# Optimization experiments

Measured on AMD Instinct MI355X. Metric: run time of the kernel, lower is better.

## Reference

```python
import jax, jax.numpy as jnp
import numpy as np

DIM = 1024
NUM_HEADS = 16
HEAD_DIM = DIM // NUM_HEADS
SCALE = HEAD_DIM ** -0.5


def setup_inputs() -> dict:
    key = jax.random.key(0)
    k1, k2, k3, k4 = jax.random.split(key, 4)
    x = jax.random.normal(k1, (4, 2048, DIM), dtype=jnp.float32)
    # torch nn.Linear(dim, 3*dim, bias=False): weight shape [3*dim, dim]
    w_qkv = jax.random.normal(k2, (3 * DIM, DIM), dtype=jnp.float32) * (DIM ** -0.5)
    # torch nn.Linear(dim, dim): weight [dim, dim], bias [dim]
    w_proj = jax.random.normal(k3, (DIM, DIM), dtype=jnp.float32) * (DIM ** -0.5)
    b_proj = jax.random.normal(k4, (DIM,), dtype=jnp.float32) * 0.01
    return {"x": x, "w_qkv": w_qkv, "w_proj": w_proj, "b_proj": b_proj}


def reference(x, w_qkv, w_proj, b_proj):
    B, N, C = x.shape
    # qkv: [B, N, 3*C] -> [3, B, H, N, Dh]
    qkv = (x @ w_qkv.T).reshape(B, N, 3, NUM_HEADS, HEAD_DIM)
    qkv = jnp.transpose(qkv, (2, 0, 3, 1, 4))
    q, k, v = qkv[0], qkv[1], qkv[2]
    # full score matrix, as in the original module
    attn = jnp.einsum("bhqd,bhkd->bhqk", q, k) * SCALE
    attn = jax.nn.softmax(attn, axis=-1)
    out = jnp.einsum("bhqk,bhkd->bhqd", attn, v)  # [B,H,N,Dh]
    out = jnp.transpose(out, (0, 2, 1, 3)).reshape(B, N, C)
    return out @ w_proj.T + b_proj
```

## Files before the change

### kernel.cpp

```cpp
#include <hip/hip_runtime.h>
#include <stdint.h>

#define DIM 1024
#define SEQ 2048
#define BATCH 4
#define ROWS (BATCH*SEQ)
#define QSCALE 0.1803368801111f

typedef __attribute__((ext_vector_type(8))) short bf16x8;
typedef __attribute__((ext_vector_type(4))) float f32x4;
typedef __attribute__((ext_vector_type(8))) _Float16 f16x8;
typedef __attribute__((ext_vector_type(2))) __fp16 fp16x2_raw;

#if __has_builtin(__builtin_amdgcn_exp2f)
#define EXP2F(x) __builtin_amdgcn_exp2f(x)
#else
#define EXP2F(x) __expf((x) * 0.69314718056f)
#endif

#define MFMA_BF16_K32(a,b,c) __builtin_amdgcn_mfma_f32_16x16x32_bf16(a,b,c,0,0,0)
#define MFMA_F16_K32(a,b,c)  __builtin_amdgcn_mfma_f32_16x16x32_f16(a,b,c,0,0,0)

__device__ __forceinline__ unsigned short f2bf(float f) {
  union { float f; unsigned int u; } v; v.f = f;
  unsigned int u = v.u;
  return (unsigned short)((u + 0x7FFFu + ((u >> 16) & 1u)) >> 16);
}

__device__ __forceinline__ unsigned short f2h(float f) {
  union { _Float16 h; unsigned short u; } v;
  v.h = (_Float16)f;
  return v.u;
}

__device__ __forceinline__ unsigned int pkrtz_bits(float lo, float hi) {
  union { fp16x2_raw h; unsigned int u; } v;
  v.h = __builtin_amdgcn_cvt_pkrtz(lo, hi);
  return v.u;
}

__device__ __forceinline__ void gload_lds16(const void* g, void* l) {
  __builtin_amdgcn_global_load_lds(
      (const __attribute__((address_space(1))) unsigned int*)g,
      (__attribute__((address_space(3))) unsigned int*)l,
      16, 0, 0);
}

__global__ void cast_all(const float* __restrict__ x,
                         const float* __restrict__ wq,
                         const float* __restrict__ wp,
                         unsigned short* __restrict__ xb,
                         unsigned short* __restrict__ wqb,
                         unsigned short* __restrict__ wpb) {
  const int i = (blockIdx.x * blockDim.x + threadIdx.x) * 4;
  const float* src;
  unsigned short* dst;
  int off;
  if (i < ROWS * DIM)                 { src = x;  dst = xb;  off = i; }
  else if (i < ROWS * DIM + 3 * DIM * DIM) { src = wq; dst = wqb; off = i - ROWS * DIM; }
  else                                { src = wp; dst = wpb; off = i - ROWS * DIM - 3 * DIM * DIM; }
  float4 f = *(const float4*)(src + off);
  ushort4 o;
  o.x = f2bf(f.x); o.y = f2bf(f.y); o.z = f2bf(f.z); o.w = f2bf(f.w);
  *(ushort4*)(dst + off) = o;
}

template<int SWAP>
__device__ __forceinline__ f32x4 mm(bf16x8 a, bf16x8 b, f32x4 c) {
  if constexpr (SWAP) return __builtin_amdgcn_mfma_f32_16x16x32_bf16(b, a, c, 0, 0, 0);
  else                return __builtin_amdgcn_mfma_f32_16x16x32_bf16(a, b, c, 0, 0, 0);
}

template<int SWAP, int NTX>
__global__ __launch_bounds__(512, 2) void gemm_qkv8(
    const unsigned short* __restrict__ A,
    const unsigned short* __restrict__ W,
    unsigned short* __restrict__ qb,
    unsigned short* __restrict__ kb,
    unsigned short* __restrict__ vtb) {
  constexpr int K = DIM;
  constexpr int NT = K / 64;
  constexpr int N0B = SWAP ? 0 : 2048;
  __shared__ unsigned short Al[2][256 * 64];
  __shared__ unsigned short Bl[2][256 * 64];

  const int tid  = threadIdx.x;
  const int wave = tid >> 6, lane = tid & 63;
  const int quad = lane >> 4, l16 = lane & 15;
  const int wm = wave >> 2, wn = wave & 3;

  constexpr int nwg = NTX * 32;
  int id = blockIdx.y * NTX + blockIdx.x;
  id = (id & 7) * (nwg >> 3) + (id >> 3);
  const int bx = id % NTX, by = id / NTX;
  const int m0 = by * 256, n0 = N0B + bx * 256;

  const int srow8 = lane >> 3;
  const int schk  = (lane & 7) ^ srow8;
  const unsigned short* Ast = A + (size_t)(m0 + wave * 8 + srow8) * K + (schk << 3);
  const unsigned short* Bst = W + (size_t)(n0 + wave * 8 + srow8) * K + (schk << 3);

  auto stg = [&](const unsigned short* g, int R0, int kt, unsigned short* l) {
    gload_lds16((const void*)(g + (size_t)R0 * K + kt),
                (void*)(l + (R0 + wave * 8) * 64));
  };
  auto ldf = [&](const unsigned short* base, int rb, int idx, int kk) -> bf16x8 {
    const int r = rb + idx * 16 + l16;
    return *(const bf16x8*)&base[r * 64 + (((kk * 4 + quad) ^ (l16 & 7)) << 3)];
  };

  f32x4 acc[8][4];
#pragma unroll
  for (int i = 0; i < 8; ++i)
#pragma unroll
    for (int j = 0; j < 4; ++j) acc[i][j] = (f32x4)0.f;

  stg(Ast, 0, 0, Al[0]);  stg(Ast, 128, 0, Al[0]);
  stg(Ast, 64, 0, Al[0]); stg(Ast, 192, 0, Al[0]);
  stg(Bst, 0, 0, Bl[0]);  stg(Bst, 64, 0, Bl[0]);
  stg(Bst, 128, 0, Bl[0]); stg(Bst, 192, 0, Bl[0]);
  stg(Ast, 0, 64, Al[1]);  stg(Ast, 128, 64, Al[1]);
  stg(Bst, 0, 64, Bl[1]);  stg(Bst, 64, 64, Bl[1]);
  stg(Ast, 64, 64, Al[1]); stg(Ast, 192, 64, Al[1]);
  asm volatile("s_waitcnt vmcnt(6)" ::: "memory");
  __builtin_amdgcn_s_barrier();

  bf16x8 af[4][2], bf[4][2];
  int buf = 0;
  for (int t = 0; t < NT; ++t, buf ^= 1) {
    const unsigned short* Ac = Al[buf];
    const unsigned short* Bc = Bl[buf];
    unsigned short* Asg = Al[buf];
    unsigned short* Bsg = Bl[buf];
    const int kt2 = (t + 2) * 64;

#pragma unroll
    for (int mi = 0; mi < 4; ++mi) {
      af[mi][0] = ldf(Ac, wm * 128, mi, 0);
      af[mi][1] = ldf(Ac, wm * 128, mi, 1);
    }
#pragma unroll
    for (int ni = 0; ni < 2; ++ni) {
      bf[ni][0] = ldf(Bc, wn * 64, ni, 0);
      bf[ni][1] = ldf(Bc, wn * 64, ni, 1);
    }
    if (t + 1 < NT) {
      stg(Bst, 128, (t + 1) * 64, Bl[buf ^ 1]);
      stg(Bst, 192, (t + 1) * 64, Bl[buf ^ 1]);
    }
    __builtin_amdgcn_s_barrier();
    asm volatile("s_waitcnt lgkmcnt(0)" ::: "memory");
    __builtin_amdgcn_s_setprio(1);
#pragma unroll
    for (int mi = 0; mi < 4; ++mi)
#pragma unroll
      for (int ni = 0; ni < 2; ++ni)
#pragma unroll
        for (int kk = 0; kk < 2; ++kk)
          acc[mi][ni] = mm<SWAP>(af[mi][kk], bf[ni][kk], acc[mi][ni]);
    __builtin_amdgcn_s_setprio(0);
    __builtin_amdgcn_s_barrier();

#pragma unroll
    for (int ni = 2; ni < 4; ++ni) {
      bf[ni][0] = ldf(Bc, wn * 64, ni, 0);
      bf[ni][1] = ldf(Bc, wn * 64, ni, 1);
    }
    if (t + 2 < NT) {
      stg(Ast, 0, kt2, Asg);
      stg(Ast, 128, kt2, Asg);
    }
    __builtin_amdgcn_s_barrier();
    asm volatile("s_waitcnt lgkmcnt(0)" ::: "memory");
    __builtin_amdgcn_s_setprio(1);
#pragma unroll
    for (int mi = 0; mi < 4; ++mi)
#pragma unroll
      for (int ni = 2; ni < 4; ++ni)
#pragma unroll
        for (int kk = 0; kk < 2; ++kk)
          acc[mi][ni] = mm<SWAP>(af[mi][kk], bf[ni][kk], acc[mi][ni]);
    __builtin_amdgcn_s_setprio(0);
    __builtin_amdgcn_s_barrier();

#pragma unroll
    for (int mi = 0; mi < 4; ++mi) {
      af[mi][0] = ldf(Ac, wm * 128, mi + 4, 0);
      af[mi][1] = ldf(Ac, wm * 128, mi + 4, 1);
    }
    if (t + 2 < NT) {
      stg(Bst, 0, kt2, Bsg);
      stg(Bst, 64, kt2, Bsg);
    }
    __builtin_amdgcn_s_barrier();
    asm volatile("s_waitcnt lgkmcnt(0)" ::: "memory");
    __builtin_amdgcn_s_setprio(1);
#pragma unroll
    for (int mi = 0; mi < 4; ++mi)
#pragma unroll
      for (int ni = 2; ni < 4; ++ni)
#pragma unroll
        for (int kk = 0; kk < 2; ++kk)
          acc[mi + 4][ni] = mm<SWAP>(af[mi][kk], bf[ni][kk], acc[mi + 4][ni]);
    __builtin_amdgcn_s_setprio(0);
    __builtin_amdgcn_s_barrier();

    if (t + 2 < NT) {
      stg(Ast, 64, kt2, Asg);
      stg(Ast, 192, kt2, Asg);
      asm volatile("s_waitcnt vmcnt(6)" ::: "memory");
    } else {
      asm volatile("s_waitcnt vmcnt(0)" ::: "memory");
    }
    __builtin_amdgcn_s_barrier();
    __builtin_amdgcn_s_setprio(1);
#pragma unroll
    for (int mi = 0; mi < 4; ++mi)
#pragma unroll
      for (int ni = 0; ni < 2; ++ni)
#pragma unroll
        for (int kk = 0; kk < 2; ++kk)
          acc[mi + 4][ni] = mm<SWAP>(af[mi][kk], bf[ni][kk], acc[mi + 4][ni]);
    __builtin_amdgcn_s_setprio(0);
    __builtin_amdgcn_s_barrier();
  }

  if constexpr (SWAP) {
    const float sc = (n0 < 1024) ? QSCALE : 1.f;
    unsigned short* base = (n0 < 1024) ? qb : kb;
#pragma unroll
    for (int mi = 0; mi < 8; ++mi) {
      const int tok = m0 + wm * 128 + mi * 16 + l16;
      const int b = tok >> 11, n = tok & 2047;
#pragma unroll
      for (int ni = 0; ni < 4; ++ni) {
        const int f0 = n0 + wn * 64 + ni * 16 + quad * 4;
        const int h = (f0 >> 6) & 15, d = f0 & 63;
        ushort4 o4;
        o4.x = f2bf(acc[mi][ni][0] * sc);
        o4.y = f2bf(acc[mi][ni][1] * sc);
        o4.z = f2bf(acc[mi][ni][2] * sc);
        o4.w = f2bf(acc[mi][ni][3] * sc);
        *(ushort4*)&base[((size_t)(b * 16 + h) * SEQ + n) * 64 + d] = o4;
      }
    }
  } else {
#pragma unroll
    for (int mi = 0; mi < 8; ++mi) {
      const int row = m0 + wm * 128 + mi * 16 + quad * 4;
      const int b = row >> 11, n = row & 2047;
#pragma unroll
      for (int ni = 0; ni < 4; ++ni) {
        const int col = n0 + wn * 64 + ni * 16 + l16;
        const int h = (col >> 6) & 15, d = col & 63;
        ushort4 o4;
        o4.x = f2h(acc[mi][ni][0]); o4.y = f2h(acc[mi][ni][1]);
        o4.z = f2h(acc[mi][ni][2]); o4.w = f2h(acc[mi][ni][3]);
        *(ushort4*)&vtb[((size_t)(b * 16 + h) * 64 + d) * SEQ + n] = o4;
      }
    }
  }
}

__global__ __launch_bounds__(256, 2) void attn_kernel(
    const unsigned short* __restrict__ qb,
    const unsigned short* __restrict__ kb,
    const unsigned short* __restrict__ vtb,
    unsigned short* __restrict__ out) {
  __shared__ unsigned short Kl[2][64 * 64];
  __shared__ unsigned short Vl[2][64 * 64];

  const int tid  = threadIdx.x;
  const int wave = tid >> 6, lane = tid & 63;
  const int quad = lane >> 4, l16 = lane & 15;
  const int bh    = blockIdx.x;
  const int qtile = blockIdx.y;
  const size_t qkbase = (size_t)bh * SEQ * 64;
  const int q0 = qtile * 256 + wave * 64;

  bf16x8 qf[4][2];
#pragma unroll
  for (int mi = 0; mi < 4; mi++)
#pragma unroll
    for (int kk = 0; kk < 2; kk++)
      qf[mi][kk] = *(const bf16x8*)&qb[qkbase + (size_t)(q0 + mi * 16 + l16) * 64 + kk * 32 + quad * 8];

  f32x4 o[4][4];
#pragma unroll
  for (int mi = 0; mi < 4; mi++)
#pragma unroll
    for (int nt = 0; nt < 4; nt++) o[mi][nt] = (f32x4)0.f;
  f32x4 lacc[4];
#pragma unroll
  for (int mi = 0; mi < 4; mi++) lacc[mi] = (f32x4)0.f;

  union { f16x8 v; unsigned int d[4]; } ones8;
#pragma unroll
  for (int j = 0; j < 4; j++) ones8.d[j] = 0x3C003C00u;

  const unsigned short* Kg = kb + qkbase;
  const unsigned short* Vg = vtb + (size_t)bh * 64 * SEQ;
  const int srow = tid >> 3;
  const int schk = tid & 7;
  const int swK = (srow & 3) | (((srow >> 3) & 1) << 2);
  const int swV = srow & 7;

  auto stage = [&](int kt, int buf) {
#pragma unroll
    for (int p = 0; p < 2; p++) {
      const int r = p * 32 + srow;
      gload_lds16((const void*)(Kg + (size_t)(kt + r) * 64 + (schk ^ swK) * 8),
                  (void*)&Kl[buf][p * 2048 + wave * 512]);
      gload_lds16((const void*)(Vg + (size_t)r * SEQ + kt + (schk ^ swV) * 8),
                  (void*)&Vl[buf][p * 2048 + wave * 512]);
    }
  };

  stage(0, 0);

  const int rbase = ((l16 >> 2) << 3) + (l16 & 3);
  const int sR = (l16 & 3) | (((l16 >> 2) & 1) << 2);

  int buf = 0;
  for (int kt = 0; kt < SEQ; kt += 64, buf ^= 1) {
    __syncthreads();
    if (kt + 64 < SEQ) stage(kt + 64, buf ^ 1);

#pragma unroll
    for (int kk = 0; kk < 2; kk++) {
      bf16x8 kf[2][2];
#pragma unroll
      for (int T = 0; T < 2; T++) {
        const int R = kk * 32 + rbase + 4 * T;
        kf[T][0] = *(const bf16x8*)&Kl[buf][R * 64 + ((quad ^ sR) << 3)];
        kf[T][1] = *(const bf16x8*)&Kl[buf][R * 64 + (((4 + quad) ^ sR) << 3)];
      }
      f16x8 vf[4];
#pragma unroll
      for (int nt = 0; nt < 4; nt++) {
        const int vr = nt * 16 + l16;
        vf[nt] = *(const f16x8*)&Vl[buf][vr * 64 + (((kk * 4 + quad) ^ (vr & 7)) << 3)];
      }
#pragma unroll
      for (int mi = 0; mi < 4; mi++) {
        f32x4 s0 = (f32x4)0.f, s1 = (f32x4)0.f;
        s0 = MFMA_BF16_K32(kf[0][0], qf[mi][0], s0);
        s0 = MFMA_BF16_K32(kf[0][1], qf[mi][1], s0);
        s1 = MFMA_BF16_K32(kf[1][0], qf[mi][0], s1);
        s1 = MFMA_BF16_K32(kf[1][1], qf[mi][1], s1);
        union { f16x8 v; unsigned int d[4]; } pu;
        pu.d[0] = pkrtz_bits(EXP2F(s0[0]), EXP2F(s0[1]));
        pu.d[1] = pkrtz_bits(EXP2F(s0[2]), EXP2F(s0[3]));
        pu.d[2] = pkrtz_bits(EXP2F(s1[0]), EXP2F(s1[1]));
        pu.d[3] = pkrtz_bits(EXP2F(s1[2]), EXP2F(s1[3]));
        lacc[mi] = MFMA_F16_K32(pu.v, ones8.v, lacc[mi]);
#pragma unroll
        for (int nt = 0; nt < 4; nt++)
          o[mi][nt] = MFMA_F16_K32(pu.v, vf[nt], o[mi][nt]);
      }
    }
  }

  const int h = bh & 15, b = bh >> 4;
#pragma unroll
  for (int mi = 0; mi < 4; mi++) {
    float inv[4];
#pragma unroll
    for (int r = 0; r < 4; r++) inv[r] = 1.f / lacc[mi][r];
#pragma unroll
    for (int nt = 0; nt < 4; nt++)
#pragma unroll
      for (int r = 0; r < 4; r++)
        out[((size_t)(b * SEQ + q0 + mi * 16 + quad * 4 + r)) * DIM + h * 64 + nt * 16 + l16] =
            f2bf(o[mi][nt][r] * inv[r]);
  }
}

__global__ __launch_bounds__(256) void gemm_proj(
    const unsigned short* __restrict__ A,
    const unsigned short* __restrict__ W,
    float* __restrict__ out,
    const float* __restrict__ bias) {
  const int N = DIM, K = DIM;
  __shared__ unsigned short Al[128 * 32];
  __shared__ unsigned short Wl[128 * 32];
  const int tid  = threadIdx.x;
  const int wave = tid >> 6, lane = tid & 63;
  const int quad = lane >> 4, l16 = lane & 15;
  const int m0 = blockIdx.y * 128, n0 = blockIdx.x * 128;
  const int wr = (wave >> 1) * 64, wc = (wave & 1) * 64;

  f32x4 acc[4][4];
#pragma unroll
  for (int i = 0; i < 4; i++)
#pragma unroll
    for (int j = 0; j < 4; j++) acc[i][j] = (f32x4)0.f;

  const int arow = wave * 16 + (lane >> 2);
  const int acol = (lane & 3) * 8;
  const unsigned short* Ag = A + (size_t)(m0 + arow) * K + acol;
  const unsigned short* Wg = W + (size_t)(n0 + arow) * K + acol;

  for (int kt = 0; kt < K; kt += 32) {
    __syncthreads();
#pragma unroll
    for (int i = 0; i < 2; i++) {
      gload_lds16((const void*)(Ag + (size_t)(i * 64) * K + kt), (void*)&Al[i * 2048 + wave * 512]);
      gload_lds16((const void*)(Wg + (size_t)(i * 64) * K + kt), (void*)&Wl[i * 2048 + wave * 512]);
    }
    __syncthreads();

    bf16x8 af[4], wf[4];
#pragma unroll
    for (int i = 0; i < 4; i++) {
      af[i] = *(const bf16x8*)&Al[(wr + i * 16 + l16) * 32 + quad * 8];
      wf[i] = *(const bf16x8*)&Wl[(wc + i * 16 + l16) * 32 + quad * 8];
    }
#pragma unroll
    for (int i = 0; i < 4; i++)
#pragma unroll
      for (int j = 0; j < 4; j++)
        acc[i][j] = __builtin_amdgcn_mfma_f32_16x16x32_bf16(af[i], wf[j], acc[i][j], 0, 0, 0);
  }

#pragma unroll
  for (int i = 0; i < 4; i++) {
    const int row = m0 + wr + i * 16 + quad * 4;
#pragma unroll
    for (int j = 0; j < 4; j++) {
      const int col = n0 + wc + j * 16 + l16;
      const float bv = bias[col];
#pragma unroll
      for (int r = 0; r < 4; r++)
        out[(size_t)(row + r) * N + col] = acc[i][j][r] + bv;
    }
  }
}

extern "C" void kernel_launch(void* const* d_in, const int* in_sizes, int n_in,
                              void* d_out, int out_size, void* d_ws, size_t ws_size,
                              hipStream_t stream) {
  const float* x      = (const float*)d_in[0];
  const float* w_qkv  = (const float*)d_in[1];
  const float* w_proj = (const float*)d_in[2];
  const float* b_proj = (const float*)d_in[3];
  float* outp = (float*)d_out;

  char* ws = (char*)d_ws;
  unsigned short* xb     = (unsigned short*)(ws);
  unsigned short* wqkvb  = (unsigned short*)(ws + (16u << 20));
  unsigned short* wprojb = (unsigned short*)(ws + (22u << 20));
  unsigned short* qb     = (unsigned short*)(ws + (24u << 20));
  unsigned short* kb     = (unsigned short*)(ws + (40u << 20));
  unsigned short* vtb    = (unsigned short*)(ws + (56u << 20));
  unsigned short* aout   = (unsigned short*)(ws + (72u << 20));

  const int total4 = (ROWS * DIM + 3 * DIM * DIM + DIM * DIM) / 4;
  cast_all<<<total4 / 256, 256, 0, stream>>>(x, w_qkv, w_proj, xb, wqkvb, wprojb);

  gemm_qkv8<1, 8><<<dim3(8, 32), 512, 0, stream>>>(xb, wqkvb, qb, kb, vtb);
  gemm_qkv8<0, 4><<<dim3(4, 32), 512, 0, stream>>>(xb, wqkvb, qb, kb, vtb);
  attn_kernel<<<dim3(64, 8), 256, 0, stream>>>(qb, kb, vtb, aout);
  gemm_proj<<<dim3(8, 64), 256, 0, stream>>>(aout, wprojb, outp, b_proj);
}
```

Measured before the change: 264.3 us.

## Add pipelined 128x256 GEMM for V and proj, use 8-wave attention blocks

Adds a new 8-wave 128x256-tile GEMM with double-buffered direct-to-LDS loads, staggered staging across four MFMA phases, and s_setprio around MFMA bursts. It replaces the old 128x128 proj GEMM and the V-part QKV GEMM. This is meant to get better reuse and overlap than the simpler single-buffer proj kernel. The attention kernel now uses 512 threads, with each wave handling 32 query rows instead of 64, which lowers register pressure and adds more waves to hide latency. The trade-off is more barriers per iteration and less per-wave reuse of K/V fragments.

Measured after the change: 257.6 us. -2.5%, faster.

```diff
diff --git a/kernel.cpp b/kernel.cpp
--- a/kernel.cpp
+++ b/kernel.cpp
@@ -262,7 +262,188 @@
   }
 }
 
-__global__ __launch_bounds__(256, 2) void attn_kernel(
+template<int EPI>
+__global__ __launch_bounds__(512, 2) void gemm8_128x256(
+    const unsigned short* __restrict__ A,
+    const unsigned short* __restrict__ W,
+    unsigned short* __restrict__ vtb,
+    float* __restrict__ outp,
+    const float* __restrict__ bias) {
+  constexpr int K = DIM;
+  constexpr int NT = K / 64;
+  __shared__ unsigned short Al[2][128 * 64];
+  __shared__ unsigned short Bl[2][256 * 64];
+
+  const int tid  = threadIdx.x;
+  const int wave = tid >> 6, lane = tid & 63;
+  const int quad = lane >> 4, l16 = lane & 15;
+  const int wm = wave >> 2, wn = wave & 3;
+
+  int id = blockIdx.y * 4 + blockIdx.x;
+  id = (id & 7) * 32 + (id >> 3);
+  const int bx = id & 3, by = id >> 2;
+  const int m0 = by * 128, n0 = bx * 256;
+
+  const int srow8 = lane >> 3;
+  const int schk  = (lane & 7) ^ srow8;
+  const unsigned short* Ast = A + (size_t)(m0 + srow8) * K + (schk << 3);
+  const unsigned short* Bst = W + (size_t)(n0 + srow8) * K + (schk << 3);
+
+  auto stgA = [&](int kt, unsigned short* l, int R0, int R1) {
+    const int rs = (wave < 4 ? R0 : R1) + (wave & 3) * 8;
+    gload_lds16((const void*)(Ast + (size_t)rs * K + kt), (void*)(l + rs * 64));
+  };
+  auto stgB = [&](int kt, unsigned short* l, int R0, int R1) {
+    const int rs = (wave < 4 ? R0 : R1) + (wave & 3) * 8;
+    gload_lds16((const void*)(Bst + (size_t)rs * K + kt), (void*)(l + rs * 64));
+  };
+  auto ldf = [&](const unsigned short* base, int rb, int idx, int kk) -> bf16x8 {
+    const int r = rb + idx * 16 + l16;
+    return *(const bf16x8*)&base[r * 64 + (((kk * 4 + quad) ^ (l16 & 7)) << 3)];
+  };
+
+  f32x4 acc[4][4];
+#pragma unroll
+  for (int i = 0; i < 4; ++i)
+#pragma unroll
+    for (int j = 0; j < 4; ++j) acc[i][j] = (f32x4)0.f;
+
+  stgA(0, Al[0], 0, 64);   stgA(0, Al[0], 32, 96);
+  stgB(0, Bl[0], 0, 64);   stgB(0, Bl[0], 32, 96);
+  stgB(0, Bl[0], 128, 192); stgB(0, Bl[0], 160, 224);
+  stgA(64, Al[1], 0, 64);  stgA(64, Al[1], 32, 96);
+  stgB(64, Bl[1], 0, 64);  stgB(64, Bl[1], 32, 96);
+  asm volatile("s_waitcnt vmcnt(4)" ::: "memory");
+  __builtin_amdgcn_s_barrier();
+
+  bf16x8 af[2][2], bf[4][2];
+  int buf = 0;
+  for (int t = 0; t < NT; ++t, buf ^= 1) {
+    const unsigned short* Ac = Al[buf];
+    const unsigned short* Bc = Bl[buf];
+    unsigned short* Asg = Al[buf];
+    unsigned short* Bsg = Bl[buf];
+    const int kt2 = (t + 2) * 64;
+
+#pragma unroll
+    for (int i = 0; i < 2; ++i) {
+      af[i][0] = ldf(Ac, wm * 64, i, 0);
+      af[i][1] = ldf(Ac, wm * 64, i, 1);
+    }
+#pragma unroll
+    for (int ni = 0; ni < 2; ++ni) {
+      bf[ni][0] = ldf(Bc, wn * 64, ni, 0);
+      bf[ni][1] = ldf(Bc, wn * 64, ni, 1);
+    }
+    if (t + 1 < NT) {
+      stgB((t + 1) * 64, Bl[buf ^ 1], 128, 192);
+      stgB((t + 1) * 64, Bl[buf ^ 1], 160, 224);
+    }
+    __builtin_amdgcn_s_barrier();
+    asm volatile("s_waitcnt lgkmcnt(0)" ::: "memory");
+    __builtin_amdgcn_s_setprio(1);
+#pragma unroll
+    for (int mi = 0; mi < 2; ++mi)
+#pragma unroll
+      for (int ni = 0; ni < 2; ++ni)
+#pragma unroll
+        for (int kk = 0; kk < 2; ++kk)
+          acc[mi][ni] = mm<0>(af[mi][kk], bf[ni][kk], acc[mi][ni]);
+    __builtin_amdgcn_s_setprio(0);
+    __builtin_amdgcn_s_barrier();
+
+#pragma unroll
+    for (int ni = 2; ni < 4; ++ni) {
+      bf[ni][0] = ldf(Bc, wn * 64, ni, 0);
+      bf[ni][1] = ldf(Bc, wn * 64, ni, 1);
+    }
+    if (t + 2 < NT) stgA(kt2, Asg, 0, 64);
+    __builtin_amdgcn_s_barrier();
+    asm volatile("s_waitcnt lgkmcnt(0)" ::: "memory");
+    __builtin_amdgcn_s_setprio(1);
+#pragma unroll
+    for (int mi = 0; mi < 2; ++mi)
+#pragma unroll
+      for (int ni = 2; ni < 4; ++ni)
+#pragma unroll
+        for (int kk = 0; kk < 2; ++kk)
+          acc[mi][ni] = mm<0>(af[mi][kk], bf[ni][kk], acc[mi][ni]);
+    __builtin_amdgcn_s_setprio(0);
+    __builtin_amdgcn_s_barrier();
+
+#pragma unroll
+    for (int i = 0; i < 2; ++i) {
+      af[i][0] = ldf(Ac, wm * 64, i + 2, 0);
+      af[i][1] = ldf(Ac, wm * 64, i + 2, 1);
+    }
+    if (t + 2 < NT) {
+      stgB(kt2, Bsg, 0, 64);
+      stgB(kt2, Bsg, 32, 96);
+    }
+    __builtin_amdgcn_s_barrier();
+    asm volatile("s_waitcnt lgkmcnt(0)" ::: "memory");
+    __builtin_amdgcn_s_setprio(1);
+#pragma unroll
+    for (int mi = 0; mi < 2; ++mi)
+#pragma unroll
+      for (int ni = 2; ni < 4; ++ni)
+#pragma unroll
+        for (int kk = 0; kk < 2; ++kk)
+          acc[mi + 2][ni] = mm<0>(af[mi][kk], bf[ni][kk], acc[mi + 2][ni]);
+    __builtin_amdgcn_s_setprio(0);
+    __builtin_amdgcn_s_barrier();
+
+    if (t + 2 < NT) {
+      stgA(kt2, Asg, 32, 96);
+      asm volatile("s_waitcnt vmcnt(4)" ::: "memory");
+    } else {
+      asm volatile("s_waitcnt vmcnt(0)" ::: "memory");
+    }
+    __builtin_amdgcn_s_barrier();
+    __builtin_amdgcn_s_setprio(1);
+#pragma unroll
+    for (int mi = 0; mi < 2; ++mi)
+#pragma unroll
+      for (int ni = 0; ni < 2; ++ni)
+#pragma unroll
+        for (int kk = 0; kk < 2; ++kk)
+          acc[mi + 2][ni] = mm<0>(af[mi][kk], bf[ni][kk], acc[mi + 2][ni]);
+    __builtin_amdgcn_s_setprio(0);
+    __builtin_amdgcn_s_barrier();
+  }
+
+  if constexpr (EPI == 0) {
+#pragma unroll
+    for (int mi = 0; mi < 4; ++mi) {
+      const int row = m0 + wm * 64 + mi * 16 + quad * 4;
+      const int b = row >> 11, n = row & 2047;
+#pragma unroll
+      for (int ni = 0; ni < 4; ++ni) {
+        const int col = n0 + wn * 64 + ni * 16 + l16;
+        const int h = (col >> 6) & 15, d = col & 63;
+        ushort4 o4;
+        o4.x = f2h(acc[mi][ni][0]); o4.y = f2h(acc[mi][ni][1]);
+        o4.z = f2h(acc[mi][ni][2]); o4.w = f2h(acc[mi][ni][3]);
+        *(ushort4*)&vtb[((size_t)(b * 16 + h) * 64 + d) * SEQ + n] = o4;
+      }
+    }
+  } else {
+#pragma unroll
+    for (int mi = 0; mi < 4; ++mi) {
+      const int row = m0 + wm * 64 + mi * 16 + quad * 4;
+#pragma unroll
+      for (int ni = 0; ni < 4; ++ni) {
+        const int col = n0 + wn * 64 + ni * 16 + l16;
+        const float bv = bias[col];
+#pragma unroll
+        for (int r = 0; r < 4; ++r)
+          outp[(size_t)(row + r) * DIM + col] = acc[mi][ni][r] + bv;
+      }
+    }
+  }
+}
+
+__global__ __launch_bounds__(512, 4) void attn_kernel(
     const unsigned short* __restrict__ qb,
     const unsigned short* __restrict__ kb,
     const unsigned short* __restrict__ vtb,
@@ -276,23 +457,23 @@
   const int bh    = blockIdx.x;
   const int qtile = blockIdx.y;
   const size_t qkbase = (size_t)bh * SEQ * 64;
-  const int q0 = qtile * 256 + wave * 64;
-
-  bf16x8 qf[4][2];
-#pragma unroll
-  for (int mi = 0; mi < 4; mi++)
+  const int q0 = qtile * 256 + wave * 32;
+
+  bf16x8 qf[2][2];
+#pragma unroll
+  for (int mi = 0; mi < 2; mi++)
 #pragma unroll
     for (int kk = 0; kk < 2; kk++)
       qf[mi][kk] = *(const bf16x8*)&qb[qkbase + (size_t)(q0 + mi * 16 + l16) * 64 + kk * 32 + quad * 8];
 
-  f32x4 o[4][4];
-#pragma unroll
-  for (int mi = 0; mi < 4; mi++)
+  f32x4 o[2][4];
+#pragma unroll
+  for (int mi = 0; mi < 2; mi++)
 #pragma unroll
     for (int nt = 0; nt < 4; nt++) o[mi][nt] = (f32x4)0.f;
-  f32x4 lacc[4];
-#pragma unroll
-  for (int mi = 0; mi < 4; mi++) lacc[mi] = (f32x4)0.f;
+  f32x4 lacc[2];
+#pragma unroll
+  for (int mi = 0; mi < 2; mi++) lacc[mi] = (f32x4)0.f;
 
   union { f16x8 v; unsigned int d[4]; } ones8;
 #pragma unroll
@@ -305,15 +486,11 @@
   const int swK = (srow & 3) | (((srow >> 3) & 1) << 2);
   const int swV = srow & 7;
 
-  auto stage = [&](int kt, int buf) {
-#pragma unroll
-    for (int p = 0; p < 2; p++) {
-      const int r = p * 32 + srow;
-      gload_lds16((const void*)(Kg + (size_t)(kt + r) * 64 + (schk ^ swK) * 8),
-                  (void*)&Kl[buf][p * 2048 + wave * 512]);
-      gload_lds16((const void*)(Vg + (size_t)r * SEQ + kt + (schk ^ swV) * 8),
-                  (void*)&Vl[buf][p * 2048 + wave * 512]);
-    }
+  auto stage = [&](int kt, int b) {
+    gload_lds16((const void*)(Kg + (size_t)(kt + srow) * 64 + (schk ^ swK) * 8),
+                (void*)&Kl[b][wave * 512]);
+    gload_lds16((const void*)(Vg + (size_t)srow * SEQ + kt + (schk ^ swV) * 8),
+                (void*)&Vl[b][wave * 512]);
   };
 
   stage(0, 0);
@@ -342,7 +519,7 @@
         vf[nt] = *(const f16x8*)&Vl[buf][vr * 64 + (((kk * 4 + quad) ^ (vr & 7)) << 3)];
       }
 #pragma unroll
-      for (int mi = 0; mi < 4; mi++) {
+      for (int mi = 0; mi < 2; mi++) {
         f32x4 s0 = (f32x4)0.f, s1 = (f32x4)0.f;
         s0 = MFMA_BF16_K32(kf[0][0], qf[mi][0], s0);
         s0 = MFMA_BF16_K32(kf[0][1], qf[mi][1], s0);
@@ -363,7 +540,7 @@
 
   const int h = bh & 15, b = bh >> 4;
 #pragma unroll
-  for (int mi = 0; mi < 4; mi++) {
+  for (int mi = 0; mi < 2; mi++) {
     float inv[4];
 #pragma unroll
     for (int r = 0; r < 4; r++) inv[r] = 1.f / lacc[mi][r];
@@ -373,67 +550,6 @@
       for (int r = 0; r < 4; r++)
         out[((size_t)(b * SEQ + q0 + mi * 16 + quad * 4 + r)) * DIM + h * 64 + nt * 16 + l16] =
             f2bf(o[mi][nt][r] * inv[r]);
-  }
-}
-
-__global__ __launch_bounds__(256) void gemm_proj(
-    const unsigned short* __restrict__ A,
-    const unsigned short* __restrict__ W,
-    float* __restrict__ out,
-    const float* __restrict__ bias) {
-  const int N = DIM, K = DIM;
-  __shared__ unsigned short Al[128 * 32];
-  __shared__ unsigned short Wl[128 * 32];
-  const int tid  = threadIdx.x;
-  const int wave = tid >> 6, lane = tid & 63;
-  const int quad = lane >> 4, l16 = lane & 15;
-  const int m0 = blockIdx.y * 128, n0 = blockIdx.x * 128;
-  const int wr = (wave >> 1) * 64, wc = (wave & 1) * 64;
-
-  f32x4 acc[4][4];
-#pragma unroll
-  for (int i = 0; i < 4; i++)
-#pragma unroll
-    for (int j = 0; j < 4; j++) acc[i][j] = (f32x4)0.f;
-
-  const int arow = wave * 16 + (lane >> 2);
-  const int acol = (lane & 3) * 8;
-  const unsigned short* Ag = A + (size_t)(m0 + arow) * K + acol;
-  const unsigned short* Wg = W + (size_t)(n0 + arow) * K + acol;
-
-  for (int kt = 0; kt < K; kt += 32) {
-    __syncthreads();
-#pragma unroll
-    for (int i = 0; i < 2; i++) {
-      gload_lds16((const void*)(Ag + (size_t)(i * 64) * K + kt), (void*)&Al[i * 2048 + wave * 512]);
-      gload_lds16((const void*)(Wg + (size_t)(i * 64) * K + kt), (void*)&Wl[i * 2048 + wave * 512]);
-    }
-    __syncthreads();
-
-    bf16x8 af[4], wf[4];
-#pragma unroll
-    for (int i = 0; i < 4; i++) {
-      af[i] = *(const bf16x8*)&Al[(wr + i * 16 + l16) * 32 + quad * 8];
-      wf[i] = *(const bf16x8*)&Wl[(wc + i * 16 + l16) * 32 + quad * 8];
-    }
-#pragma unroll
-    for (int i = 0; i < 4; i++)
-#pragma unroll
-      for (int j = 0; j < 4; j++)
-        acc[i][j] = __builtin_amdgcn_mfma_f32_16x16x32_bf16(af[i], wf[j], acc[i][j], 0, 0, 0);
-  }
-
-#pragma unroll
-  for (int i = 0; i < 4; i++) {
-    const int row = m0 + wr + i * 16 + quad * 4;
-#pragma unroll
-    for (int j = 0; j < 4; j++) {
-      const int col = n0 + wc + j * 16 + l16;
-      const float bv = bias[col];
-#pragma unroll
-      for (int r = 0; r < 4; r++)
-        out[(size_t)(row + r) * N + col] = acc[i][j][r] + bv;
-    }
   }
 }
 
@@ -459,7 +575,9 @@
   cast_all<<<total4 / 256, 256, 0, stream>>>(x, w_qkv, w_proj, xb, wqkvb, wprojb);
 
   gemm_qkv8<1, 8><<<dim3(8, 32), 512, 0, stream>>>(xb, wqkvb, qb, kb, vtb);
-  gemm_qkv8<0, 4><<<dim3(4, 32), 512, 0, stream>>>(xb, wqkvb, qb, kb, vtb);
-  attn_kernel<<<dim3(64, 8), 256, 0, stream>>>(qb, kb, vtb, aout);
-  gemm_proj<<<dim3(8, 64), 256, 0, stream>>>(aout, wprojb, outp, b_proj);
-}
+  gemm8_128x256<0><<<dim3(4, 64), 512, 0, stream>>>(
+      xb, wqkvb + (size_t)2048 * DIM, vtb, nullptr, nullptr);
+  attn_kernel<<<dim3(64, 8), 512, 0, stream>>>(qb, kb, vtb, aout);
+  gemm8_128x256<1><<<dim3(4, 64), 512, 0, stream>>>(
+      aout, wprojb, nullptr, outp, b_proj);
+}
```
